# Kernel optimization log

Hardware: AMD Instinct MI355X
Metric: run time of the kernel (lower is better)

Reference implementation:

```python
import jax, jax.numpy as jnp
import numpy as np

B, S, D, H = 2, 2048, 1024, 16
DH = D // H          # 64, even -> RoPE valid
ROPE_BASE = 10000.0
LN_EPS = 1e-5


def _rope_cache(seq_len, head_dim, dtype):
    half = head_dim // 2
    inv_freq = 1.0 / (ROPE_BASE ** (jnp.arange(half, dtype=jnp.float32) / half))
    t = jnp.arange(seq_len, dtype=jnp.float32)
    freqs = t[:, None] * inv_freq[None, :]            # [S, half]
    emb = jnp.concatenate([freqs, freqs], axis=-1)    # [S, DH]
    return jnp.cos(emb).astype(dtype)[None, None], jnp.sin(emb).astype(dtype)[None, None]


def _rotate_every_two(x):
    x_even = x[..., ::2]
    x_odd = x[..., 1::2]
    return jnp.stack([-x_odd, x_even], axis=-1).reshape(x.shape)


def setup_inputs() -> dict:
    key = jax.random.key(0)
    ks = jax.random.split(key, 4)
    w = lambda k, shape: (jax.random.normal(k, shape, jnp.float32) * 0.02)
    return {
        "x_qk": jax.random.normal(ks[0], (B, S, D), jnp.float32),
        "x_v": jax.random.normal(ks[1], (B, S, D), jnp.float32),
        "W_qk": w(ks[2], (D, 2 * D)),
        "b_qk": jnp.zeros((2 * D,), jnp.float32),
        "W_v": w(ks[3], (D, D)),
        "b_v": jnp.zeros((D,), jnp.float32),
        "ln_gamma": jnp.ones((D,), jnp.float32),
        "ln_beta": jnp.zeros((D,), jnp.float32),
    }


def reference(x_qk, x_v, W_qk, b_qk, W_v, b_v, ln_gamma, ln_beta):
    b, s, d = x_qk.shape
    # fused QK projection -> [B,S,2,H,DH]
    qk = (x_qk @ W_qk + b_qk).reshape(b, s, 2, H, DH)
    q = jnp.transpose(qk[:, :, 0], (0, 2, 1, 3))  # [B,H,S,DH]
    k = jnp.transpose(qk[:, :, 1], (0, 2, 1, 3))
    v = jnp.transpose((x_v @ W_v + b_v).reshape(b, s, H, DH), (0, 2, 1, 3))

    cos, sin = _rope_cache(s, DH, q.dtype)
    q = q * cos + _rotate_every_two(q) * sin
    k = k * cos + _rotate_every_two(k) * sin

    scale = 1.0 / jnp.sqrt(jnp.asarray(DH, q.dtype))
    scores = jnp.einsum("bhqd,bhkd->bhqk", q, k) * scale
    probs = jax.nn.softmax(scores, axis=-1)
    attn = jnp.einsum("bhqk,bhkd->bhqd", probs, v)      # [B,H,S,DH]
    attn = jnp.transpose(attn, (0, 2, 1, 3)).reshape(b, s, d)

    mu = jnp.mean(attn, axis=-1, keepdims=True)
    var = jnp.var(attn, axis=-1, keepdims=True)
    out = (attn - mu) * jax.lax.rsqrt(var + LN_EPS) * ln_gamma + ln_beta
    return out
```

## Files before the change

### kernel.cpp

```cpp
#include <hip/hip_runtime.h>
#include <hip/hip_bf16.h>

#define Bn 2
#define Sn 2048
#define Dn 1024
#define Hn 16
#define DHn 64
#define Kd 1024
#define Mn (Bn * Sn)
#define LN10K 9.210340371976184f

typedef __attribute__((ext_vector_type(8))) short bf16x8;
typedef __attribute__((ext_vector_type(4))) float f32x4;

static __device__ __forceinline__ ushort f2bf(float f) {
    uint u = __float_as_uint(f);
    u += 0x7fff + ((u >> 16) & 1);
    return (ushort)(u >> 16);
}
static __device__ __forceinline__ uint cvtpk(float a, float b) {
    uint r;
    asm("v_cvt_pk_bf16_f32 %0, %1, %2" : "=v"(r) : "v"(a), "v"(b));
    return r;
}

#define MFMA16(a, b, c) __builtin_amdgcn_mfma_f32_16x16x32_bf16((a), (b), (c), 0, 0, 0)

static __device__ __forceinline__ void gload16(const ushort* g, ushort* l) {
    __builtin_amdgcn_global_load_lds(
        (const __attribute__((address_space(1))) void*)g,
        (__attribute__((address_space(3))) void*)l, 16, 0, 0);
}

static __device__ __forceinline__ int swz(int row, int col16) {
    return row * 128 + (((col16) * 16) ^ ((row & 7) << 4));
}

__global__ __launch_bounds__(256) void rope_tab(float* __restrict__ ct,
                                                float* __restrict__ st)
{
    const int idx = blockIdx.x * 256 + threadIdx.x;
    const int s = idx >> 5, fe = idx & 31;
    const float f = expf(-LN10K * (float)fe / 32.0f);
    const float a = (float)s * f;
    ct[idx] = cosf(a);
    st[idx] = sinf(a);
}

__global__ __launch_bounds__(256) void cvt_bf16(const float* __restrict__ in,
                                                ushort* __restrict__ out)
{
    const size_t i = ((size_t)blockIdx.x * 256 + threadIdx.x) * 8;
    const float4 a = *(const float4*)(in + i);
    const float4 b = *(const float4*)(in + i + 4);
    ushort4 lo = make_ushort4(f2bf(a.x), f2bf(a.y), f2bf(a.z), f2bf(a.w));
    ushort4 hi = make_ushort4(f2bf(b.x), f2bf(b.y), f2bf(b.z), f2bf(b.w));
    *(ushort4*)(out + i) = lo;
    *(ushort4*)(out + i + 4) = hi;
}

__global__ __launch_bounds__(256) void transpose_bf16(
    const float* __restrict__ in, ushort* __restrict__ out, int R, int C)
{
    __shared__ ushort t[32][33];
    const int n0 = blockIdx.x * 32, k0 = blockIdx.y * 32;
    const int x = threadIdx.x, y = threadIdx.y;
#pragma unroll
    for (int i = 0; i < 4; ++i)
        t[y + 8 * i][x] = f2bf(in[(size_t)(k0 + y + 8 * i) * C + n0 + x]);
    __syncthreads();
#pragma unroll
    for (int i = 0; i < 4; ++i)
        out[(size_t)(n0 + y + 8 * i) * R + k0 + x] = t[x][y + 8 * i];
}

template <int MODE>
__global__ __launch_bounds__(256) void gemm_mfma(
    const ushort* __restrict__ A, const ushort* __restrict__ Bt,
    const float* __restrict__ bias, const float* __restrict__ ctab,
    const float* __restrict__ stab, ushort* __restrict__ o0,
    ushort* __restrict__ o1)
{
    __shared__ ushort Asm[128 * 64];
    __shared__ ushort Bsm[128 * 64];

    const int tid = threadIdx.x;
    const int lane = tid & 63, w = tid >> 6;
    const int g = lane >> 4, c = lane & 15;
    const int mbase = blockIdx.y * 128;
    const int nbase = blockIdx.x * 128;
    const int wm = (w >> 1) * 64, wn = (w & 1) * 64;

    f32x4 acc[4][4];
#pragma unroll
    for (int mf = 0; mf < 4; ++mf)
#pragma unroll
        for (int nf = 0; nf < 4; ++nf)
            acc[mf][nf] = (f32x4){0.f, 0.f, 0.f, 0.f};

    const int sbase = w * 64 + lane;

    for (int k0 = 0; k0 < Kd; k0 += 64) {
#pragma unroll
        for (int j = 0; j < 4; ++j) {
            const int i = j * 256 + sbase;
            const int row = i >> 3, c16 = i & 7;
            const int kc = (c16 ^ (row & 7)) * 8;
            gload16(A + (size_t)(mbase + row) * Kd + k0 + kc,
                    &Asm[(size_t)(j * 256 + w * 64) * 8]);
            gload16(Bt + (size_t)(nbase + row) * Kd + k0 + kc,
                    &Bsm[(size_t)(j * 256 + w * 64) * 8]);
        }
        __syncthreads();

#pragma unroll
        for (int ks = 0; ks < 2; ++ks) {
            bf16x8 af[4], bfr[4];
#pragma unroll
            for (int mf = 0; mf < 4; ++mf) {
                const int row = wm + mf * 16 + c;
                af[mf] = *(const bf16x8*)((const char*)Asm + swz(row, ks * 4 + g));
            }
#pragma unroll
            for (int nf = 0; nf < 4; ++nf) {
                const int row = wn + nf * 16 + c;
                bfr[nf] = *(const bf16x8*)((const char*)Bsm + swz(row, ks * 4 + g));
            }
#pragma unroll
            for (int mf = 0; mf < 4; ++mf)
#pragma unroll
                for (int nf = 0; nf < 4; ++nf)
                    acc[mf][nf] = MFMA16(af[mf], bfr[nf], acc[mf][nf]);
        }
        __syncthreads();
    }

#pragma unroll
    for (int nf = 0; nf < 4; ++nf) {
        const int col = nbase + wn + nf * 16 + c;
        const float bs = bias[col];
        if (MODE == 0) {
            const int dh = col & 63, h = (col >> 6) & 15, isK = col >> 10;
            ushort* dst = isK ? o1 : o0;
            const float sc = isK ? 1.0f : 0.125f;
            const float* cr = ctab + (dh & 31);
            const float* sr = stab + (dh & 31);
#pragma unroll
            for (int mf = 0; mf < 4; ++mf) {
#pragma unroll
                for (int r = 0; r < 4; ++r) {
                    const int row = mbase + wm + mf * 16 + g * 4 + r;
                    const int s = row & 2047, b = row >> 11;
                    const float v = acc[mf][nf][r] + bs;
                    const float p = __shfl_xor(v, 1);
                    const float cs = cr[s * 32], sn = sr[s * 32];
                    const float ov = (c & 1) ? v * cs + p * sn
                                             : v * cs - p * sn;
                    dst[(((size_t)(b * Hn + h)) * Sn + s) * DHn + dh] =
                        f2bf(ov * sc);
                }
            }
        } else {
            const int h = col >> 6, dh = col & 63;
#pragma unroll
            for (int mf = 0; mf < 4; ++mf) {
#pragma unroll
                for (int r = 0; r < 4; ++r) {
                    const int row = mbase + wm + mf * 16 + g * 4 + r;
                    const int s = row & 2047, b = row >> 11;
                    const float v = acc[mf][nf][r] + bs;
                    o0[(((size_t)(b * Hn + h)) * DHn + dh) * Sn + s] = f2bf(v);
                }
            }
        }
    }
}

__global__ __launch_bounds__(256) void attn_mfma(
    const ushort* __restrict__ Qg, const ushort* __restrict__ Kg,
    const ushort* __restrict__ Vtg, float* __restrict__ Aw)
{
    __shared__ char Kt[2][8192];
    __shared__ char Vt[2][8192];

    const int tid = threadIdx.x;
    const int lane = tid & 63, w = tid >> 6;
    const int g = lane >> 4, c = lane & 15;
    const int bh = blockIdx.y;
    const int b = bh >> 4, h = bh & 15;
    const int q0 = blockIdx.x * 64 + w * 16;

    const size_t qrow = ((size_t)bh * Sn + q0 + c) * DHn;
    const bf16x8 qa0 = *(const bf16x8*)&Qg[qrow + g * 8];
    const bf16x8 qa1 = *(const bf16x8*)&Qg[qrow + 32 + g * 8];

    const ushort* Kb = Kg + (size_t)bh * Sn * DHn;
    const ushort* Vb = Vtg + (size_t)bh * DHn * Sn;

    auto stage = [&](int buf, int kb) {
#pragma unroll
        for (int j = 0; j < 2; ++j) {
            const int i = j * 256 + w * 64 + lane;
            const int row = i >> 3, c16 = i & 7;
            const int kc = (c16 ^ (row & 7)) * 8;
            gload16(Kb + (size_t)(kb + row) * DHn + kc,
                    (ushort*)&Kt[buf][(j * 256 + w * 64) * 16]);
            gload16(Vb + (size_t)row * Sn + kb + kc,
                    (ushort*)&Vt[buf][(j * 256 + w * 64) * 16]);
        }
    };

    stage(0, 0);
    __syncthreads();

    f32x4 acc[4];
#pragma unroll
    for (int nf = 0; nf < 4; ++nf) acc[nf] = (f32x4){0.f, 0.f, 0.f, 0.f};
    float m = -1e30f, lp = 0.f;

    for (int t = 0; t < Sn / 64; ++t) {
        const int cur = t & 1;
        if (t + 1 < Sn / 64) stage(cur ^ 1, (t + 1) * 64);

        const f32x4 z = {0.f, 0.f, 0.f, 0.f};
        f32x4 C[4];
        __builtin_amdgcn_s_setprio(1);
#pragma unroll
        for (int sub = 0; sub < 4; ++sub) {
            const bf16x8 k0 = *(const bf16x8*)&Kt[cur][swz(sub * 16 + c, g)];
            const bf16x8 k1 = *(const bf16x8*)&Kt[cur][swz(sub * 16 + c, 4 + g)];
            C[sub] = MFMA16(k0, qa0, z);
            C[sub] = MFMA16(k1, qa1, C[sub]);
        }
        __builtin_amdgcn_s_setprio(0);

        float pmax = fmaxf(fmaxf(C[0][0], C[0][1]), fmaxf(C[0][2], C[0][3]));
        pmax = fmaxf(pmax, fmaxf(fmaxf(C[1][0], C[1][1]), fmaxf(C[1][2], C[1][3])));
        pmax = fmaxf(pmax, fmaxf(fmaxf(C[2][0], C[2][1]), fmaxf(C[2][2], C[2][3])));
        pmax = fmaxf(pmax, fmaxf(fmaxf(C[3][0], C[3][1]), fmaxf(C[3][2], C[3][3])));
        pmax = fmaxf(pmax, __shfl_xor(pmax, 16));
        pmax = fmaxf(pmax, __shfl_xor(pmax, 32));

        if (__any(pmax > m + 8.0f)) {
            const float mn = fmaxf(m, pmax);
            const float a = __expf(m - mn);
            m = mn;
            lp *= a;
            float ar[4];
#pragma unroll
            for (int r = 0; r < 4; ++r) ar[r] = __shfl(a, g * 4 + r);
#pragma unroll
            for (int nf = 0; nf < 4; ++nf)
#pragma unroll
                for (int r = 0; r < 4; ++r) acc[nf][r] *= ar[r];
        }

        uint pk[4][2];
        float s0 = 0.f, s1 = 0.f;
#pragma unroll
        for (int sub = 0; sub < 4; ++sub) {
            const float e0 = __expf(C[sub][0] - m);
            const float e1 = __expf(C[sub][1] - m);
            const float e2 = __expf(C[sub][2] - m);
            const float e3 = __expf(C[sub][3] - m);
            s0 += e0 + e1;
            s1 += e2 + e3;
            pk[sub][0] = cvtpk(e0, e1);
            pk[sub][1] = cvtpk(e2, e3);
        }
        lp += s0 + s1;

#pragma unroll
        for (int half = 0; half < 2; ++half) {
            const int x0 = (int)pk[2 * half][0], x1 = (int)pk[2 * half][1];
            const int x2 = (int)pk[2 * half + 1][0], x3 = (int)pk[2 * half + 1][1];
            const int sA = ((g & 1) * 2) * 16 + c;
            const int sB = sA + 16;
            const uint u0 = (uint)__shfl(x0, sA), u1 = (uint)__shfl(x1, sA);
            const uint u2 = (uint)__shfl(x2, sA), u3 = (uint)__shfl(x3, sA);
            const uint v0 = (uint)__shfl(x0, sB), v1 = (uint)__shfl(x1, sB);
            const uint v2 = (uint)__shfl(x2, sB), v3 = (uint)__shfl(x3, sB);
            const bool hb = (g >> 1) != 0;
            uint4 fu;
            fu.x = hb ? u2 : u0;
            fu.y = hb ? u3 : u1;
            fu.z = hb ? v2 : v0;
            fu.w = hb ? v3 : v1;
            const bf16x8 pa = *(const bf16x8*)&fu;
            __builtin_amdgcn_s_setprio(1);
#pragma unroll
            for (int nf = 0; nf < 4; ++nf) {
                const bf16x8 vf =
                    *(const bf16x8*)&Vt[cur][swz(nf * 16 + c, half * 4 + g)];
                acc[nf] = MFMA16(pa, vf, acc[nf]);
            }
            __builtin_amdgcn_s_setprio(0);
        }

        __syncthreads();
    }

    float lv = lp;
    lv += __shfl_xor(lv, 16);
    lv += __shfl_xor(lv, 32);
#pragma unroll
    for (int r = 0; r < 4; ++r) {
        const float inv = 1.0f / __shfl(lv, g * 4 + r);
        const int qs = q0 + g * 4 + r;
        float* dst = &Aw[((size_t)b * Sn + qs) * Dn + h * DHn + c];
        dst[0]  = acc[0][r] * inv;
        dst[16] = acc[1][r] * inv;
        dst[32] = acc[2][r] * inv;
        dst[48] = acc[3][r] * inv;
    }
}

__global__ __launch_bounds__(256) void ln_kernel(
    const float* __restrict__ Aw, const float* __restrict__ gamma,
    const float* __restrict__ beta, float* __restrict__ out)
{
    const int row = blockIdx.x;
    const int tid = threadIdx.x;
    const int d0 = tid * 4;
    const float4 x = *(const float4*)&Aw[(size_t)row * Dn + d0];
    float sum = x.x + x.y + x.z + x.w;
    float sq = x.x * x.x + x.y * x.y + x.z * x.z + x.w * x.w;
    for (int off = 32; off; off >>= 1) {
        sum += __shfl_xor(sum, off);
        sq += __shfl_xor(sq, off);
    }
    __shared__ float red[8];
    const int lane = tid & 63, wave = tid >> 6;
    if (lane == 0) { red[wave] = sum; red[wave + 4] = sq; }
    __syncthreads();
    if (tid == 0) {
        red[0] = red[0] + red[1] + red[2] + red[3];
        red[4] = red[4] + red[5] + red[6] + red[7];
    }
    __syncthreads();
    sum = red[0]; sq = red[4];
    const float mu = sum * (1.0f / Dn);
    const float var = sq * (1.0f / Dn) - mu * mu;
    const float rs = rsqrtf(var + 1e-5f);

    const float4 gv = *(const float4*)&gamma[d0];
    const float4 bv = *(const float4*)&beta[d0];
    float4 ov;
    ov.x = (x.x - mu) * rs * gv.x + bv.x;
    ov.y = (x.y - mu) * rs * gv.y + bv.y;
    ov.z = (x.z - mu) * rs * gv.z + bv.z;
    ov.w = (x.w - mu) * rs * gv.w + bv.w;
    *(float4*)&out[(size_t)row * Dn + d0] = ov;
}

extern "C" void kernel_launch(void* const* d_in, const int* in_sizes, int n_in,
                              void* d_out, int out_size, void* d_ws, size_t ws_size,
                              hipStream_t stream)
{
    const float* x_qk = (const float*)d_in[0];
    const float* x_v  = (const float*)d_in[1];
    const float* W_qk = (const float*)d_in[2];
    const float* b_qk = (const float*)d_in[3];
    const float* W_v  = (const float*)d_in[4];
    const float* b_v  = (const float*)d_in[5];
    const float* g    = (const float*)d_in[6];
    const float* be   = (const float*)d_in[7];

    char* ws = (char*)d_ws;
    ushort* Qw    = (ushort*)(ws);
    ushort* Kw    = (ushort*)(ws + (8u  << 20));
    ushort* Vtw   = (ushort*)(ws + (16u << 20));
    float*  Aw    = (float*) (ws + (24u << 20));
    ushort* xqkB  = (ushort*)(ws + (40u << 20));
    ushort* xvB   = (ushort*)(ws + (48u << 20));
    ushort* WqkT  = (ushort*)(ws + (56u << 20));
    ushort* WvT   = (ushort*)(ws + (60u << 20));
    float*  ctab  = (float*) (ws + (62u << 20));
    float*  stab  = (float*) (ws + (62u << 20) + (256u << 10));

    rope_tab<<<256, 256, 0, stream>>>(ctab, stab);
    cvt_bf16<<<2048, 256, 0, stream>>>(x_qk, xqkB);
    cvt_bf16<<<2048, 256, 0, stream>>>(x_v, xvB);
    transpose_bf16<<<dim3(64, 32), dim3(32, 8), 0, stream>>>(W_qk, WqkT, Kd, 2048);
    transpose_bf16<<<dim3(32, 32), dim3(32, 8), 0, stream>>>(W_v, WvT, Kd, 1024);

    gemm_mfma<0><<<dim3(16, 32), 256, 0, stream>>>(
        xqkB, WqkT, b_qk, ctab, stab, Qw, Kw);
    gemm_mfma<1><<<dim3(8, 32), 256, 0, stream>>>(
        xvB, WvT, b_v, ctab, stab, Vtw, nullptr);

    attn_mfma<<<dim3(32, 32), 256, 0, stream>>>(Qw, Kw, Vtw, Aw);
    ln_kernel<<<Bn * Sn, 256, 0, stream>>>(Aw, g, be, (float*)d_out);
}
```

Measured before the change: 171.2 us.

## Rewrite attention with 32x32x16 MFMA tiles, exp2 softmax and permlane swap

The attention kernel now uses 32x32x16 bf16 MFMAs, with each wave owning 32 query rows, so a block covers 128 queries and the grid halves. The log2(e) factor is folded into the Q scale so the softmax can use exp2f. The P fragment is rebuilt with v_permlane32_swap instead of many shuffles, and the rescale threshold is raised to match the base-2 scale. This aims to cut shuffle and LDS-read overhead and reload K/V less often per query, at the cost of more accumulator registers and fewer blocks.

```diff
diff --git a/kernel.cpp b/kernel.cpp
--- a/kernel.cpp
+++ b/kernel.cpp
@@ -12,6 +12,7 @@
 
 typedef __attribute__((ext_vector_type(8))) short bf16x8;
 typedef __attribute__((ext_vector_type(4))) float f32x4;
+typedef __attribute__((ext_vector_type(16))) float f32x16;
 
 static __device__ __forceinline__ ushort f2bf(float f) {
     uint u = __float_as_uint(f);
@@ -23,8 +24,12 @@
     asm("v_cvt_pk_bf16_f32 %0, %1, %2" : "=v"(r) : "v"(a), "v"(b));
     return r;
 }
+static __device__ __forceinline__ void plswap(uint& a, uint& b) {
+    asm volatile("v_permlane32_swap_b32 %0, %1" : "+v"(a), "+v"(b));
+}
 
 #define MFMA16(a, b, c) __builtin_amdgcn_mfma_f32_16x16x32_bf16((a), (b), (c), 0, 0, 0)
+#define MFMA32(a, b, c) __builtin_amdgcn_mfma_f32_32x32x16_bf16((a), (b), (c), 0, 0, 0)
 
 static __device__ __forceinline__ void gload16(const ushort* g, ushort* l) {
     __builtin_amdgcn_global_load_lds(
@@ -142,7 +147,7 @@
         if (MODE == 0) {
             const int dh = col & 63, h = (col >> 6) & 15, isK = col >> 10;
             ushort* dst = isK ? o1 : o0;
-            const float sc = isK ? 1.0f : 0.125f;
+            const float sc = isK ? 1.0f : 0.18033688011112042f;
             const float* cr = ctab + (dh & 31);
             const float* sr = stab + (dh & 31);
 #pragma unroll
@@ -185,14 +190,16 @@
 
     const int tid = threadIdx.x;
     const int lane = tid & 63, w = tid >> 6;
-    const int g = lane >> 4, c = lane & 15;
+    const int r31 = lane & 31, hi = lane >> 5;
     const int bh = blockIdx.y;
     const int b = bh >> 4, h = bh & 15;
-    const int q0 = blockIdx.x * 64 + w * 16;
-
-    const size_t qrow = ((size_t)bh * Sn + q0 + c) * DHn;
-    const bf16x8 qa0 = *(const bf16x8*)&Qg[qrow + g * 8];
-    const bf16x8 qa1 = *(const bf16x8*)&Qg[qrow + 32 + g * 8];
+    const int q0 = blockIdx.x * 128 + w * 32;
+
+    const ushort* qp = Qg + ((size_t)bh * Sn + q0 + r31) * DHn + hi * 8;
+    bf16x8 qf[4];
+#pragma unroll
+    for (int kt = 0; kt < 4; ++kt)
+        qf[kt] = *(const bf16x8*)(qp + kt * 16);
 
     const ushort* Kb = Kg + (size_t)bh * Sn * DHn;
     const ushort* Vb = Vtg + (size_t)bh * DHn * Sn;
@@ -213,105 +220,103 @@
     stage(0, 0);
     __syncthreads();
 
-    f32x4 acc[4];
-#pragma unroll
-    for (int nf = 0; nf < 4; ++nf) acc[nf] = (f32x4){0.f, 0.f, 0.f, 0.f};
+    f32x16 acc0, acc1;
+#pragma unroll
+    for (int i = 0; i < 16; ++i) { acc0[i] = 0.f; acc1[i] = 0.f; }
     float m = -1e30f, lp = 0.f;
 
     for (int t = 0; t < Sn / 64; ++t) {
         const int cur = t & 1;
         if (t + 1 < Sn / 64) stage(cur ^ 1, (t + 1) * 64);
 
-        const f32x4 z = {0.f, 0.f, 0.f, 0.f};
-        f32x4 C[4];
+        f32x16 C0, C1;
+#pragma unroll
+        for (int i = 0; i < 16; ++i) { C0[i] = 0.f; C1[i] = 0.f; }
         __builtin_amdgcn_s_setprio(1);
 #pragma unroll
-        for (int sub = 0; sub < 4; ++sub) {
-            const bf16x8 k0 = *(const bf16x8*)&Kt[cur][swz(sub * 16 + c, g)];
-            const bf16x8 k1 = *(const bf16x8*)&Kt[cur][swz(sub * 16 + c, 4 + g)];
-            C[sub] = MFMA16(k0, qa0, z);
-            C[sub] = MFMA16(k1, qa1, C[sub]);
+        for (int kt = 0; kt < 4; ++kt) {
+            const bf16x8 ka = *(const bf16x8*)&Kt[cur][swz(r31, kt * 2 + hi)];
+            C0 = MFMA32(ka, qf[kt], C0);
+        }
+#pragma unroll
+        for (int kt = 0; kt < 4; ++kt) {
+            const bf16x8 ka = *(const bf16x8*)&Kt[cur][swz(32 + r31, kt * 2 + hi)];
+            C1 = MFMA32(ka, qf[kt], C1);
         }
         __builtin_amdgcn_s_setprio(0);
 
-        float pmax = fmaxf(fmaxf(C[0][0], C[0][1]), fmaxf(C[0][2], C[0][3]));
-        pmax = fmaxf(pmax, fmaxf(fmaxf(C[1][0], C[1][1]), fmaxf(C[1][2], C[1][3])));
-        pmax = fmaxf(pmax, fmaxf(fmaxf(C[2][0], C[2][1]), fmaxf(C[2][2], C[2][3])));
-        pmax = fmaxf(pmax, fmaxf(fmaxf(C[3][0], C[3][1]), fmaxf(C[3][2], C[3][3])));
-        pmax = fmaxf(pmax, __shfl_xor(pmax, 16));
+        float mx[8];
+#pragma unroll
+        for (int i = 0; i < 8; ++i)
+            mx[i] = fmaxf(fmaxf(C0[i], C0[i + 8]), fmaxf(C1[i], C1[i + 8]));
+        mx[0] = fmaxf(mx[0], mx[4]); mx[1] = fmaxf(mx[1], mx[5]);
+        mx[2] = fmaxf(mx[2], mx[6]); mx[3] = fmaxf(mx[3], mx[7]);
+        float pmax = fmaxf(fmaxf(mx[0], mx[1]), fmaxf(mx[2], mx[3]));
         pmax = fmaxf(pmax, __shfl_xor(pmax, 32));
 
-        if (__any(pmax > m + 8.0f)) {
+        if (__any(pmax > m + 11.5f)) {
             const float mn = fmaxf(m, pmax);
-            const float a = __expf(m - mn);
+            const float a = exp2f(m - mn);
             m = mn;
             lp *= a;
-            float ar[4];
-#pragma unroll
-            for (int r = 0; r < 4; ++r) ar[r] = __shfl(a, g * 4 + r);
-#pragma unroll
-            for (int nf = 0; nf < 4; ++nf)
-#pragma unroll
-                for (int r = 0; r < 4; ++r) acc[nf][r] *= ar[r];
-        }
-
-        uint pk[4][2];
-        float s0 = 0.f, s1 = 0.f;
-#pragma unroll
-        for (int sub = 0; sub < 4; ++sub) {
-            const float e0 = __expf(C[sub][0] - m);
-            const float e1 = __expf(C[sub][1] - m);
-            const float e2 = __expf(C[sub][2] - m);
-            const float e3 = __expf(C[sub][3] - m);
-            s0 += e0 + e1;
-            s1 += e2 + e3;
-            pk[sub][0] = cvtpk(e0, e1);
-            pk[sub][1] = cvtpk(e2, e3);
-        }
-        lp += s0 + s1;
-
-#pragma unroll
-        for (int half = 0; half < 2; ++half) {
-            const int x0 = (int)pk[2 * half][0], x1 = (int)pk[2 * half][1];
-            const int x2 = (int)pk[2 * half + 1][0], x3 = (int)pk[2 * half + 1][1];
-            const int sA = ((g & 1) * 2) * 16 + c;
-            const int sB = sA + 16;
-            const uint u0 = (uint)__shfl(x0, sA), u1 = (uint)__shfl(x1, sA);
-            const uint u2 = (uint)__shfl(x2, sA), u3 = (uint)__shfl(x3, sA);
-            const uint v0 = (uint)__shfl(x0, sB), v1 = (uint)__shfl(x1, sB);
-            const uint v2 = (uint)__shfl(x2, sB), v3 = (uint)__shfl(x3, sB);
-            const bool hb = (g >> 1) != 0;
-            uint4 fu;
-            fu.x = hb ? u2 : u0;
-            fu.y = hb ? u3 : u1;
-            fu.z = hb ? v2 : v0;
-            fu.w = hb ? v3 : v1;
-            const bf16x8 pa = *(const bf16x8*)&fu;
-            __builtin_amdgcn_s_setprio(1);
-#pragma unroll
-            for (int nf = 0; nf < 4; ++nf) {
-                const bf16x8 vf =
-                    *(const bf16x8*)&Vt[cur][swz(nf * 16 + c, half * 4 + g)];
-                acc[nf] = MFMA16(pa, vf, acc[nf]);
-            }
-            __builtin_amdgcn_s_setprio(0);
-        }
+#pragma unroll
+            for (int reg = 0; reg < 16; ++reg) {
+                const int qr = (reg & 3) + 8 * (reg >> 2) + 4 * hi;
+                const float ar = __shfl(a, qr);
+                acc0[reg] *= ar;
+                acc1[reg] *= ar;
+            }
+        }
+
+        bf16x8 paf[4];
+#pragma unroll
+        for (int tile = 0; tile < 2; ++tile) {
+            const f32x16& C = tile ? C1 : C0;
+            float e[16];
+#pragma unroll
+            for (int i = 0; i < 16; ++i) e[i] = exp2f(C[i] - m);
+            float s = 0.f;
+#pragma unroll
+            for (int i = 0; i < 16; ++i) s += e[i];
+            lp += s;
+            uint p01 = cvtpk(e[0], e[1]),  p23 = cvtpk(e[2], e[3]);
+            uint p45 = cvtpk(e[4], e[5]),  p67 = cvtpk(e[6], e[7]);
+            uint p89 = cvtpk(e[8], e[9]),  pab = cvtpk(e[10], e[11]);
+            uint pcd = cvtpk(e[12], e[13]), pef = cvtpk(e[14], e[15]);
+            plswap(p01, p45); plswap(p23, p67);
+            plswap(p89, pcd); plswap(pab, pef);
+            uint4 f0 = {p01, p23, p45, p67};
+            uint4 f1 = {p89, pab, pcd, pef};
+            paf[tile * 2 + 0] = *(const bf16x8*)&f0;
+            paf[tile * 2 + 1] = *(const bf16x8*)&f1;
+        }
+
+        __builtin_amdgcn_s_setprio(1);
+#pragma unroll
+        for (int kf = 0; kf < 4; ++kf) {
+            const bf16x8 v0 = *(const bf16x8*)&Vt[cur][swz(r31, kf * 2 + hi)];
+            acc0 = MFMA32(paf[kf], v0, acc0);
+        }
+#pragma unroll
+        for (int kf = 0; kf < 4; ++kf) {
+            const bf16x8 v1 = *(const bf16x8*)&Vt[cur][swz(32 + r31, kf * 2 + hi)];
+            acc1 = MFMA32(paf[kf], v1, acc1);
+        }
+        __builtin_amdgcn_s_setprio(0);
 
         __syncthreads();
     }
 
-    float lv = lp;
-    lv += __shfl_xor(lv, 16);
-    lv += __shfl_xor(lv, 32);
-#pragma unroll
-    for (int r = 0; r < 4; ++r) {
-        const float inv = 1.0f / __shfl(lv, g * 4 + r);
-        const int qs = q0 + g * 4 + r;
-        float* dst = &Aw[((size_t)b * Sn + qs) * Dn + h * DHn + c];
-        dst[0]  = acc[0][r] * inv;
-        dst[16] = acc[1][r] * inv;
-        dst[32] = acc[2][r] * inv;
-        dst[48] = acc[3][r] * inv;
+    const float lv = lp + __shfl_xor(lp, 32);
+    const float inv = 1.0f / lv;
+#pragma unroll
+    for (int reg = 0; reg < 16; ++reg) {
+        const int qr = (reg & 3) + 8 * (reg >> 2) + 4 * hi;
+        const float ir = __shfl(inv, qr);
+        const int qs = q0 + qr;
+        float* dst = &Aw[((size_t)b * Sn + qs) * Dn + h * DHn + r31];
+        dst[0]  = acc0[reg] * ir;
+        dst[32] = acc1[reg] * ir;
     }
 }
 
@@ -389,6 +394,6 @@
     gemm_mfma<1><<<dim3(8, 32), 256, 0, stream>>>(
         xvB, WvT, b_v, ctab, stab, Vtw, nullptr);
 
-    attn_mfma<<<dim3(32, 32), 256, 0, stream>>>(Qw, Kw, Vtw, Aw);
+    attn_mfma<<<dim3(16, 32), 256, 0, stream>>>(Qw, Kw, Vtw, Aw);
     ln_kernel<<<Bn * Sn, 256, 0, stream>>>(Aw, g, be, (float*)d_out);
 }
```

After: 171.9 us. About the same (+0.4%).
